# Kernel optimization log

Measured on AMD Instinct MI355X. Metric: run time of the kernel, lower is better.

## Reference

```python
import jax, jax.numpy as jnp
import numpy as np
from jax import lax

L = 2  # layer_nums (fixed per init_kwargs)

def setup_inputs() -> dict:
    key = jax.random.key(0)
    ks = jax.random.split(key, 8)
    B, T, V, E, U = 2048, 80, 10000, 100, 256
    tokens = jax.random.randint(ks[0], (B, T), 0, V, dtype=jnp.int32)
    emb = jax.random.normal(ks[1], (V, E), dtype=jnp.float32) * 0.05
    Wx0 = jax.random.normal(ks[2], (E, U), dtype=jnp.float32) * (1.0 / np.sqrt(E))
    Wx1 = jax.random.normal(ks[3], (U, U), dtype=jnp.float32) * (1.0 / np.sqrt(U))
    Wh = jax.random.normal(ks[4], (L, U, U), dtype=jnp.float32) * (1.0 / np.sqrt(U))
    b = jnp.zeros((L, U), dtype=jnp.float32)
    h0 = jax.random.uniform(ks[5], (L, B, U), dtype=jnp.float32)  # tf.random.uniform init states
    Wo = jax.random.normal(ks[6], (U, 1), dtype=jnp.float32) * (1.0 / np.sqrt(U))
    bo = jnp.zeros((1,), dtype=jnp.float32)
    return {"tokens": tokens, "emb": emb, "Wx0": Wx0, "Wx1": Wx1,
            "Wh": Wh, "b": b, "h0": h0, "Wo": Wo, "bo": bo}

def reference(tokens, emb, Wx0, Wx1, Wh, b, h0, Wo, bo):
    # Embedding lookup: [B, T] -> [B, T, E]
    x = emb[tokens]
    xT = jnp.swapaxes(x, 0, 1)  # [T, B, E] for time-major scan
    Wxs = [Wx0, Wx1]

    def step(h, xt):
        # h: [L, B, U]; xt: [B, E]
        inp = xt
        new_h = []
        for i in range(L):
            hi = jnp.tanh(inp @ Wxs[i] + h[i] @ Wh[i] + b[i])
            new_h.append(hi)
            inp = hi
        return jnp.stack(new_h), None

    hT, _ = lax.scan(step, h0, xT)
    out = hT[-1]                      # last layer's hidden at final timestep [B, U]
    z = out @ Wo + bo                 # Dense(1)
    return jax.nn.sigmoid(z)          # [B, 1]
```

## Files before the change

kernel.cpp:

```cpp
#include <hip/hip_runtime.h>
#include <hip/hip_bf16.h>

typedef __bf16 bf16x8 __attribute__((ext_vector_type(8)));
typedef __bf16 bf16x4 __attribute__((ext_vector_type(4)));
typedef float  f32x4  __attribute__((ext_vector_type(4)));

#define MFMA16(a,b,c) __builtin_amdgcn_mfma_f32_16x16x32_bf16((a),(b),(c),0,0,0)

#define PIN8(v8) do { f32x4 _t = __builtin_bit_cast(f32x4, (v8)); \
                      asm volatile("" : "+v"(_t)); \
                      (v8) = __builtin_bit_cast(bf16x8, _t); } while (0)

__device__ __forceinline__ void barrier_lds() {
  asm volatile("s_waitcnt lgkmcnt(0)\n\ts_barrier" ::: "memory");
}

constexpr int Bb = 2048, Tt = 80, Ee = 100, Uu = 256;
constexpr int BM = 8;
constexpr int RNT = 512;
constexpr int HCH = 256;
constexpr int HB = 8 * HCH;

template<bool ISBF>
__device__ __forceinline__ float ldf(const void* p, int i) {
  if constexpr (ISBF) return (float)((const __bf16*)p)[i];
  else                return ((const float*)p)[i];
}

__device__ __forceinline__ float fast_tanh(float x) {
  float e = __expf(2.f * x);
  return 1.f - 2.f / (e + 1.f);
}

__device__ __forceinline__ bool detect_bf16(const void* wh) {
  const unsigned short* u = (const unsigned short*)wh;
  int c = 0;
  const int lane = threadIdx.x & 63;
  #pragma unroll
  for (int r = 0; r < 4; ++r) {
    unsigned short h = u[2 * (lane + 64 * r)];
    int ex = (h >> 7) & 0xFF;
    if (ex >= 135 || (ex >= 1 && ex <= 95)) c++;
  }
  #pragma unroll
  for (int o = 32; o >= 1; o >>= 1) c += __shfl_down(c, o, 64);
  return __shfl(c, 0, 64) < 64;
}

template<bool ISBF>
__launch_bounds__(RNT, 2)
__global__ void rnn_kernel(const int* __restrict__ tokens,
                           const void* __restrict__ emb,
                           const void* __restrict__ Wx0,
                           const void* __restrict__ Wx1,
                           const void* __restrict__ Wh,
                           const void* __restrict__ bias,
                           const void* __restrict__ h0g,
                           const void* __restrict__ Wo,
                           const void* __restrict__ bo,
                           __bf16* __restrict__ U,
                           void* __restrict__ out) {
  if (detect_bf16(Wh) != ISBF) return;

  __shared__ __align__(16) __bf16 s_h0[2 * HB];
  __shared__ __align__(16) __bf16 s_h1[2 * HB];
  __shared__ int s_tok[BM * Tt];

  const int tid = threadIdx.x, lane = tid & 63, wv = tid >> 6;
  const int m = lane & 15, kc = lane >> 4, hf = lane >> 5;
  const int rb = blockIdx.x, b0 = rb * BM;
  const int au = (kc * 8 + (m & 7)) * 8;

  for (int idx = tid; idx < BM * Tt; idx += RNT)
    s_tok[idx] = tokens[b0 * Tt + idx];

  for (int idx = tid; idx < BM * Uu; idx += RNT) {
    int r = idx >> 8, c = idx & 255;
    int off = (c >> 5) * HCH + (((c >> 3) & 3) * 8 + r) * 8 + (c & 7);
    s_h0[off] = (__bf16)ldf<ISBF>(h0g, (b0 + r) * Uu + c);
    s_h1[off] = (__bf16)ldf<ISBF>(h0g, Bb * Uu + (b0 + r) * Uu + c);
  }
  __syncthreads();

  {
    bf16x8 fX[2][4];
    float b0v[2];
    #pragma unroll
    for (int e = 0; e < 2; ++e) {
      const int col = wv * 32 + e * 16 + m;
      b0v[e] = ldf<ISBF>(bias, col);
      #pragma unroll
      for (int s = 0; s < 4; ++s) {
        bf16x8 tr;
        #pragma unroll
        for (int j = 0; j < 8; ++j) {
          int k = s * 32 + kc * 8 + j;
          tr[j] = (k < Ee) ? (__bf16)ldf<ISBF>(Wx0, k * Uu + col) : (__bf16)0.f;
        }
        fX[e][s] = tr;
      }
    }
    const int tid32p = (wv >> 1) * 32 + (kc & 1) * 16 + m;
    __bf16* Ustore = U + (size_t)tid32p * 16 + (wv & 1) * 8;
    for (int tc = 0; tc < 10; ++tc) {
      const int T0 = tc * 8;
      bf16x8 xa[4][4];
      #pragma unroll
      for (int mt = 0; mt < 4; ++mt) {
        const int tok = s_tok[(m & 7) * Tt + T0 + mt * 2 + (m >> 3)];
        #pragma unroll
        for (int s = 0; s < 4; ++s) {
          const int k0 = s * 32 + kc * 8;
          if (k0 + 8 <= Ee) {
            if constexpr (ISBF) {
              xa[mt][s] = *(const bf16x8*)((const __bf16*)emb + tok * Ee + k0);
            } else {
              f32x4 lo = *(const f32x4*)((const float*)emb + tok * Ee + k0);
              f32x4 hi = *(const f32x4*)((const float*)emb + tok * Ee + k0 + 4);
              #pragma unroll
              for (int j = 0; j < 4; ++j) { xa[mt][s][j] = (__bf16)lo[j]; xa[mt][s][4 + j] = (__bf16)hi[j]; }
            }
          } else if (k0 < Ee) {
            if constexpr (ISBF) {
              bf16x4 t4 = *(const bf16x4*)((const __bf16*)emb + tok * Ee + k0);
              #pragma unroll
              for (int j = 0; j < 4; ++j) { xa[mt][s][j] = t4[j]; xa[mt][s][4 + j] = (__bf16)0.f; }
            } else {
              f32x4 t4 = *(const f32x4*)((const float*)emb + tok * Ee + k0);
              #pragma unroll
              for (int j = 0; j < 4; ++j) { xa[mt][s][j] = (__bf16)t4[j]; xa[mt][s][4 + j] = (__bf16)0.f; }
            }
          } else {
            #pragma unroll
            for (int j = 0; j < 8; ++j) xa[mt][s][j] = (__bf16)0.f;
          }
        }
      }
      #pragma unroll
      for (int mt = 0; mt < 4; ++mt) {
        f32x4 a0 = {b0v[0], b0v[0], b0v[0], b0v[0]};
        f32x4 a1 = {b0v[1], b0v[1], b0v[1], b0v[1]};
        #pragma unroll
        for (int s = 0; s < 4; ++s) {
          a0 = MFMA16(xa[mt][s], fX[0][s], a0);
          a1 = MFMA16(xa[mt][s], fX[1][s], a1);
        }
        bf16x8 pk;
        #pragma unroll
        for (int i = 0; i < 4; ++i) { pk[i] = (__bf16)a0[i]; pk[4 + i] = (__bf16)a1[i]; }
        const int t_l = T0 + mt * 2 + (kc >> 1);
        *(bf16x8*)(Ustore + (size_t)(t_l * 256 + rb) * 2048) = pk;
      }
    }
  }

  bf16x8 fWh0[2][8], fWx1f[2][8], fWh1[2][8];
  #pragma unroll
  for (int e = 0; e < 2; ++e) {
    const int col = wv * 32 + e * 16 + m;
    #pragma unroll
    for (int s = 0; s < 8; ++s) {
      const int kb = s * 32 + kc * 8;
      bf16x8 t0, t1, t2;
      #pragma unroll
      for (int j = 0; j < 8; ++j) {
        t0[j] = (__bf16)ldf<ISBF>(Wh,  (kb + j) * Uu + col);
        t1[j] = (__bf16)ldf<ISBF>(Wx1, (kb + j) * Uu + col);
        t2[j] = (__bf16)ldf<ISBF>(Wh,  Uu * Uu + (kb + j) * Uu + col);
      }
      fWh0[e][s] = t0; fWx1f[e][s] = t1; fWh1[e][s] = t2;
    }
  }
  #pragma unroll
  for (int e = 0; e < 2; ++e) {
    #pragma unroll
    for (int s = 0; s < 8; ++s) {
      PIN8(fWh0[e][s]); PIN8(fWx1f[e][s]); PIN8(fWh1[e][s]);
    }
  }
  const float b1s = ldf<ISBF>(bias, Uu + wv * 32 + hf * 16 + m);

  const int tid32u = (wv >> 1) * 32 + ((kc & 1) * 16) + m;
  const __bf16* Ubase = U + (size_t)tid32u * 16 + (wv & 1) * 8 + (size_t)rb * 2048;

  const int kc2 = m >> 3, j2 = m & 7, rgr = ((lane >> 4) & 1) * 4;
  const int toffw = wv * HCH + ((hf * 2 + kc2) * 8 + rgr) * 8 + j2;

  __syncthreads();

  bf16x8 u0 = *(const bf16x8*)(Ubase);

  {
    f32x4 d0 = {(float)u0[0], (float)u0[1], (float)u0[2], (float)u0[3]};
    f32x4 d1 = {(float)u0[4], (float)u0[5], (float)u0[6], (float)u0[7]};
    const __bf16* hb = s_h0 + au;
    #pragma unroll
    for (int s = 0; s < 8; ++s) {
      bf16x8 a = *(const bf16x8*)(hb + s * HCH);
      d0 = MFMA16(a, fWh0[0][s], d0);
      d1 = MFMA16(a, fWh0[1][s], d1);
    }
    u0 = *(const bf16x8*)(Ubase + (size_t)1 * 256 * 2048);
    __bf16* wp = s_h0 + HB + toffw;
    #pragma unroll
    for (int ii = 0; ii < 4; ++ii) {
      float dd = hf ? d1[ii] : d0[ii];
      wp[ii * 8] = (__bf16)fast_tanh(dd);
    }
    barrier_lds();
  }

  for (int t = 0; t < Tt; ++t) {
    const int p = t & 1, pn = p ^ 1;
    int tf = (t + 2 < Tt) ? t + 2 : Tt - 1;
    bf16x8 un = *(const bf16x8*)(Ubase + (size_t)tf * 256 * 2048);

    f32x4 cB0 = {0.f,0.f,0.f,0.f}, cB1 = {0.f,0.f,0.f,0.f};
    f32x4 cC0 = {0.f,0.f,0.f,0.f}, cC1 = {0.f,0.f,0.f,0.f};
    f32x4 cD0 = {(float)u0[0], (float)u0[1], (float)u0[2], (float)u0[3]};
    f32x4 cD1 = {(float)u0[4], (float)u0[5], (float)u0[6], (float)u0[7]};
    {
      const __bf16* h0b = s_h0 + pn * HB + au;
      const __bf16* h1b = s_h1 + p * HB + au;
      #pragma unroll
      for (int s = 0; s < 8; ++s) {
        bf16x8 a0 = *(const bf16x8*)(h0b + s * HCH);
        bf16x8 a1 = *(const bf16x8*)(h1b + s * HCH);
        cB0 = MFMA16(a0, fWx1f[0][s], cB0);
        cB1 = MFMA16(a0, fWx1f[1][s], cB1);
        cD0 = MFMA16(a0, fWh0[0][s], cD0);
        cD1 = MFMA16(a0, fWh0[1][s], cD1);
        cC0 = MFMA16(a1, fWh1[0][s], cC0);
        cC1 = MFMA16(a1, fWh1[1][s], cC1);
      }
    }
    {
      __bf16* wp1 = s_h1 + pn * HB + toffw;
      __bf16* wp0 = s_h0 + p * HB + toffw;
      #pragma unroll
      for (int ii = 0; ii < 4; ++ii) {
        float v1 = hf ? (cB1[ii] + cC1[ii]) : (cB0[ii] + cC0[ii]);
        float v0 = hf ? cD1[ii] : cD0[ii];
        wp1[ii * 8] = (__bf16)fast_tanh(v1 + b1s);
        wp0[ii * 8] = (__bf16)fast_tanh(v0);
      }
    }
    u0 = un;
    barrier_lds();
  }

  if (tid < 256) {
    const int r = tid >> 5, q = tid & 31;
    const __bf16* hp = s_h1 + (q >> 2) * HCH + ((q & 3) * 8 + r) * 8;
    bf16x8 hv = *(const bf16x8*)hp;
    float part = 0.f;
    #pragma unroll
    for (int j = 0; j < 8; ++j) part += (float)hv[j] * ldf<ISBF>(Wo, q * 8 + j);
    #pragma unroll
    for (int o = 16; o >= 1; o >>= 1) part += __shfl_down(part, o, 32);
    if (q == 0) {
      float z = part + ldf<ISBF>(bo, 0);
      float sg = 1.f / (1.f + __expf(-z));
      if constexpr (ISBF) ((__bf16*)out)[b0 + r] = (__bf16)sg;
      else                ((float*)out)[b0 + r]  = sg;
    }
  }
}

extern "C" void kernel_launch(void* const* d_in, const int* in_sizes, int n_in,
                              void* d_out, int out_size, void* d_ws, size_t ws_size,
                              hipStream_t stream) {
  const int*  tokens = (const int*)d_in[0];
  const void* emb = d_in[1];
  const void* Wx0 = d_in[2];
  const void* Wx1 = d_in[3];
  const void* Wh  = d_in[4];
  const void* b   = d_in[5];
  const void* h0  = d_in[6];
  const void* Wo  = d_in[7];
  const void* bo  = d_in[8];

  __bf16* U = (__bf16*)((char*)d_ws + 256);
  const size_t needU = 256 + (size_t)Tt * 256 * 2048 * sizeof(__bf16);
  if (ws_size < needU) return;

  rnn_kernel<true ><<<dim3(Bb / BM), dim3(RNT), 0, stream>>>(
      tokens, emb, Wx0, Wx1, Wh, b, h0, Wo, bo, U, d_out);
  rnn_kernel<false><<<dim3(Bb / BM), dim3(RNT), 0, stream>>>(
      tokens, emb, Wx0, Wx1, Wh, b, h0, Wo, bo, U, d_out);
}
```

Baseline: 243.1 us.

## Split recurrent step across 16 waves with permlane32 swap to combine partial results

Doubles the block to 1024 threads so each wave owns 16 output columns instead of 32, halving register-resident weight fragments per wave. Within a wave, lanes with m<8 and m>=8 read different hidden states (layer0 vs layer1). v_permlane32_swap exchanges the partial accumulators between half-waves so one half finalizes layer-1 and the other layer-0. This is meant to cut per-wave serial MFMA chain length and register pressure in the latency-bound recurrence. The cost is more waves per barrier, the extra permutes, and a runtime probe of permlane semantics.

New measurement: 333.5 us. 37.2% more time.

```diff
diff --git a/kernel.cpp b/kernel.cpp
--- a/kernel.cpp
+++ b/kernel.cpp
@@ -17,7 +17,7 @@
 
 constexpr int Bb = 2048, Tt = 80, Ee = 100, Uu = 256;
 constexpr int BM = 8;
-constexpr int RNT = 512;
+constexpr int RNT = 1024;
 constexpr int HCH = 256;
 constexpr int HB = 8 * HCH;
 
@@ -48,7 +48,7 @@
 }
 
 template<bool ISBF>
-__launch_bounds__(RNT, 2)
+__launch_bounds__(RNT)
 __global__ void rnn_kernel(const int* __restrict__ tokens,
                            const void* __restrict__ emb,
                            const void* __restrict__ Wx0,
@@ -68,8 +68,13 @@
 
   const int tid = threadIdx.x, lane = tid & 63, wv = tid >> 6;
   const int m = lane & 15, kc = lane >> 4, hf = lane >> 5;
+  const int mh = (m >> 3) & 1;
   const int rb = blockIdx.x, b0 = rb * BM;
-  const int au = (kc * 8 + (m & 7)) * 8;
+  const int au2 = (kc * 8 + (m & 7)) * 8;
+
+  int pv = lane, qv = 64 + lane;
+  asm volatile("v_permlane32_swap_b32 %0, %1" : "+v"(pv), "+v"(qv));
+  const bool forma = (__shfl(pv, 0, 64) == 0);
 
   for (int idx = tid; idx < BM * Tt; idx += RNT)
     s_tok[idx] = tokens[b0 * Tt + idx];
@@ -82,7 +87,7 @@
   }
   __syncthreads();
 
-  {
+  if (wv < 8) {
     bf16x8 fX[2][4];
     float b0v[2];
     #pragma unroll
@@ -154,10 +159,10 @@
     }
   }
 
-  bf16x8 fWh0[2][8], fWx1f[2][8], fWh1[2][8];
-  #pragma unroll
-  for (int e = 0; e < 2; ++e) {
-    const int col = wv * 32 + e * 16 + m;
+  const int tw = wv;
+  bf16x8 fWh0[8], fWx1f[8], fWh1[8];
+  {
+    const int col = tw * 16 + m;
     #pragma unroll
     for (int s = 0; s < 8; ++s) {
       const int kb = s * 32 + kc * 8;
@@ -168,44 +173,38 @@
         t1[j] = (__bf16)ldf<ISBF>(Wx1, (kb + j) * Uu + col);
         t2[j] = (__bf16)ldf<ISBF>(Wh,  Uu * Uu + (kb + j) * Uu + col);
       }
-      fWh0[e][s] = t0; fWx1f[e][s] = t1; fWh1[e][s] = t2;
+      fWh0[s] = t0; fWx1f[s] = t1; fWh1[s] = t2;
     }
   }
   #pragma unroll
-  for (int e = 0; e < 2; ++e) {
+  for (int s = 0; s < 8; ++s) { PIN8(fWh0[s]); PIN8(fWx1f[s]); PIN8(fWh1[s]); }
+
+  const float b1s = ldf<ISBF>(bias, Uu + tw * 16 + m);
+
+  const int O0u = (tw >> 2) * 512 + (kc & 1) * 256 + m * 16 +
+                  ((tw >> 1) & 1) * 8 + (tw & 1) * 4;
+  const __bf16* Ubase = U + (size_t)rb * 2048 + O0u;
+
+  const int woff = (tw >> 1) * 256 +
+                   ((((tw * 2) + (m >> 3)) & 3) * 8 + (kc & 1) * 4) * 8 + (m & 7);
+
+  __syncthreads();
+
+  bf16x4 u0 = *(const bf16x4*)(Ubase);
+
+  {
+    f32x4 d = {(float)u0[0], (float)u0[1], (float)u0[2], (float)u0[3]};
+    const __bf16* ab = (mh ? s_h1 : s_h0) + au2;
     #pragma unroll
     for (int s = 0; s < 8; ++s) {
-      PIN8(fWh0[e][s]); PIN8(fWx1f[e][s]); PIN8(fWh1[e][s]);
-    }
-  }
-  const float b1s = ldf<ISBF>(bias, Uu + wv * 32 + hf * 16 + m);
-
-  const int tid32u = (wv >> 1) * 32 + ((kc & 1) * 16) + m;
-  const __bf16* Ubase = U + (size_t)tid32u * 16 + (wv & 1) * 8 + (size_t)rb * 2048;
-
-  const int kc2 = m >> 3, j2 = m & 7, rgr = ((lane >> 4) & 1) * 4;
-  const int toffw = wv * HCH + ((hf * 2 + kc2) * 8 + rgr) * 8 + j2;
-
-  __syncthreads();
-
-  bf16x8 u0 = *(const bf16x8*)(Ubase);
-
-  {
-    f32x4 d0 = {(float)u0[0], (float)u0[1], (float)u0[2], (float)u0[3]};
-    f32x4 d1 = {(float)u0[4], (float)u0[5], (float)u0[6], (float)u0[7]};
-    const __bf16* hb = s_h0 + au;
-    #pragma unroll
-    for (int s = 0; s < 8; ++s) {
-      bf16x8 a = *(const bf16x8*)(hb + s * HCH);
-      d0 = MFMA16(a, fWh0[0][s], d0);
-      d1 = MFMA16(a, fWh0[1][s], d1);
-    }
-    u0 = *(const bf16x8*)(Ubase + (size_t)1 * 256 * 2048);
-    __bf16* wp = s_h0 + HB + toffw;
-    #pragma unroll
-    for (int ii = 0; ii < 4; ++ii) {
-      float dd = hf ? d1[ii] : d0[ii];
-      wp[ii * 8] = (__bf16)fast_tanh(dd);
+      bf16x8 a = *(const bf16x8*)(ab + s * HCH);
+      d = MFMA16(a, fWh0[s], d);
+    }
+    u0 = *(const bf16x4*)(Ubase + (size_t)1 * 256 * 2048);
+    if (hf == 0) {
+      __bf16* wp = s_h0 + HB + woff;
+      #pragma unroll
+      for (int ii = 0; ii < 4; ++ii) wp[ii * 8] = (__bf16)fast_tanh(d[ii]);
     }
     barrier_lds();
   }
@@ -213,37 +212,28 @@
   for (int t = 0; t < Tt; ++t) {
     const int p = t & 1, pn = p ^ 1;
     int tf = (t + 2 < Tt) ? t + 2 : Tt - 1;
-    bf16x8 un = *(const bf16x8*)(Ubase + (size_t)tf * 256 * 2048);
-
-    f32x4 cB0 = {0.f,0.f,0.f,0.f}, cB1 = {0.f,0.f,0.f,0.f};
-    f32x4 cC0 = {0.f,0.f,0.f,0.f}, cC1 = {0.f,0.f,0.f,0.f};
-    f32x4 cD0 = {(float)u0[0], (float)u0[1], (float)u0[2], (float)u0[3]};
-    f32x4 cD1 = {(float)u0[4], (float)u0[5], (float)u0[6], (float)u0[7]};
-    {
-      const __bf16* h0b = s_h0 + pn * HB + au;
-      const __bf16* h1b = s_h1 + p * HB + au;
-      #pragma unroll
-      for (int s = 0; s < 8; ++s) {
-        bf16x8 a0 = *(const bf16x8*)(h0b + s * HCH);
-        bf16x8 a1 = *(const bf16x8*)(h1b + s * HCH);
-        cB0 = MFMA16(a0, fWx1f[0][s], cB0);
-        cB1 = MFMA16(a0, fWx1f[1][s], cB1);
-        cD0 = MFMA16(a0, fWh0[0][s], cD0);
-        cD1 = MFMA16(a0, fWh0[1][s], cD1);
-        cC0 = MFMA16(a1, fWh1[0][s], cC0);
-        cC1 = MFMA16(a1, fWh1[1][s], cC1);
-      }
-    }
-    {
-      __bf16* wp1 = s_h1 + pn * HB + toffw;
-      __bf16* wp0 = s_h0 + p * HB + toffw;
-      #pragma unroll
-      for (int ii = 0; ii < 4; ++ii) {
-        float v1 = hf ? (cB1[ii] + cC1[ii]) : (cB0[ii] + cC0[ii]);
-        float v0 = hf ? cD1[ii] : cD0[ii];
-        wp1[ii * 8] = (__bf16)fast_tanh(v1 + b1s);
-        wp0[ii * 8] = (__bf16)fast_tanh(v0);
-      }
+    bf16x4 un = *(const bf16x4*)(Ubase + (size_t)tf * 256 * 2048);
+
+    const __bf16* ab = (mh ? (s_h1 + p * HB) : (s_h0 + pn * HB)) + au2;
+
+    f32x4 accX = {0.f, 0.f, 0.f, 0.f}, accH = {0.f, 0.f, 0.f, 0.f};
+    f32x4 accD = {(float)u0[0], (float)u0[1], (float)u0[2], (float)u0[3]};
+    #pragma unroll
+    for (int s = 0; s < 8; ++s) {
+      bf16x8 a = *(const bf16x8*)(ab + s * HCH);
+      accX = MFMA16(a, fWx1f[s], accX);
+      accH = MFMA16(a, fWh1[s], accH);
+      accD = MFMA16(a, fWh0[s], accD);
+    }
+
+    __bf16* wpw = (hf ? (s_h0 + p * HB) : (s_h1 + pn * HB)) + woff;
+    #pragma unroll
+    for (int i = 0; i < 4; ++i) {
+      float hx = accH[i], dx = accD[i];
+      if (forma) asm volatile("v_permlane32_swap_b32 %0, %1" : "+v"(hx), "+v"(dx));
+      else       asm volatile("v_permlane32_swap_b32 %0, %1" : "+v"(dx), "+v"(hx));
+      float v = hf ? hx : (accX[i] + dx + b1s);
+      wpw[i * 8] = (__bf16)fast_tanh(v);
     }
     u0 = un;
     barrier_lds();
```

## Split MFMA rows between h0/h1 sources and exchange results via permlane32 swap

Applied to the files above, without the earlier changes.

Each wave now uses the MFMA row dimension for both layers at once. Lanes with m<8 read the layer-0 hidden state and lanes with m>=8 read the layer-1 hidden state, so one LDS A-operand load per k-step feeds all six MFMAs instead of two separate loads. Partial results for the two layers are then exchanged between half-waves with v_permlane32_swap_b32, and each half-wave writes tanh outputs for one layer. This halves the LDS reads per step and balances the tanh/store work across lanes. In exchange it adds cross-lane swaps, a runtime probe of the swap semantics, and more complex index math.

Result: slower. 260.0 us (+7.0%).

```diff
diff --git a/kernel.cpp b/kernel.cpp
--- a/kernel.cpp
+++ b/kernel.cpp
@@ -68,8 +68,13 @@
 
   const int tid = threadIdx.x, lane = tid & 63, wv = tid >> 6;
   const int m = lane & 15, kc = lane >> 4, hf = lane >> 5;
+  const int mh = (m >> 3) & 1;
   const int rb = blockIdx.x, b0 = rb * BM;
-  const int au = (kc * 8 + (m & 7)) * 8;
+  const int au2 = (kc * 8 + (m & 7)) * 8;
+
+  int pv = lane, qv = 64 + lane;
+  asm volatile("v_permlane32_swap_b32 %0, %1" : "+v"(pv), "+v"(qv));
+  const bool forma = (__shfl(pv, 0, 64) == 0);
 
   for (int idx = tid; idx < BM * Tt; idx += RNT)
     s_tok[idx] = tokens[b0 * Tt + idx];
@@ -178,13 +183,19 @@
       PIN8(fWh0[e][s]); PIN8(fWx1f[e][s]); PIN8(fWh1[e][s]);
     }
   }
-  const float b1s = ldf<ISBF>(bias, Uu + wv * 32 + hf * 16 + m);
+  float b1v[2];
+  b1v[0] = ldf<ISBF>(bias, Uu + wv * 32 + m);
+  b1v[1] = ldf<ISBF>(bias, Uu + wv * 32 + 16 + m);
 
   const int tid32u = (wv >> 1) * 32 + ((kc & 1) * 16) + m;
   const __bf16* Ubase = U + (size_t)tid32u * 16 + (wv & 1) * 8 + (size_t)rb * 2048;
 
-  const int kc2 = m >> 3, j2 = m & 7, rgr = ((lane >> 4) & 1) * 4;
-  const int toffw = wv * HCH + ((hf * 2 + kc2) * 8 + rgr) * 8 + j2;
+  int woffe[2];
+  #pragma unroll
+  for (int e = 0; e < 2; ++e) {
+    const int col = (wv * 2 + e) * 16 + m;
+    woffe[e] = (col >> 5) * HCH + ((((col >> 3) & 3) * 8) + (kc & 1) * 4) * 8 + (col & 7);
+  }
 
   __syncthreads();
 
@@ -193,19 +204,20 @@
   {
     f32x4 d0 = {(float)u0[0], (float)u0[1], (float)u0[2], (float)u0[3]};
     f32x4 d1 = {(float)u0[4], (float)u0[5], (float)u0[6], (float)u0[7]};
-    const __bf16* hb = s_h0 + au;
+    const __bf16* ab = (mh ? s_h1 : s_h0) + au2;
     #pragma unroll
     for (int s = 0; s < 8; ++s) {
-      bf16x8 a = *(const bf16x8*)(hb + s * HCH);
+      bf16x8 a = *(const bf16x8*)(ab + s * HCH);
       d0 = MFMA16(a, fWh0[0][s], d0);
       d1 = MFMA16(a, fWh0[1][s], d1);
     }
     u0 = *(const bf16x8*)(Ubase + (size_t)1 * 256 * 2048);
-    __bf16* wp = s_h0 + HB + toffw;
-    #pragma unroll
-    for (int ii = 0; ii < 4; ++ii) {
-      float dd = hf ? d1[ii] : d0[ii];
-      wp[ii * 8] = (__bf16)fast_tanh(dd);
+    if (hf == 0) {
+      #pragma unroll
+      for (int ii = 0; ii < 4; ++ii) {
+        (s_h0 + HB + woffe[0])[ii * 8] = (__bf16)fast_tanh(d0[ii]);
+        (s_h0 + HB + woffe[1])[ii * 8] = (__bf16)fast_tanh(d1[ii]);
+      }
     }
     barrier_lds();
   }
@@ -215,35 +227,41 @@
     int tf = (t + 2 < Tt) ? t + 2 : Tt - 1;
     bf16x8 un = *(const bf16x8*)(Ubase + (size_t)tf * 256 * 2048);
 
-    f32x4 cB0 = {0.f,0.f,0.f,0.f}, cB1 = {0.f,0.f,0.f,0.f};
-    f32x4 cC0 = {0.f,0.f,0.f,0.f}, cC1 = {0.f,0.f,0.f,0.f};
-    f32x4 cD0 = {(float)u0[0], (float)u0[1], (float)u0[2], (float)u0[3]};
-    f32x4 cD1 = {(float)u0[4], (float)u0[5], (float)u0[6], (float)u0[7]};
-    {
-      const __bf16* h0b = s_h0 + pn * HB + au;
-      const __bf16* h1b = s_h1 + p * HB + au;
-      #pragma unroll
-      for (int s = 0; s < 8; ++s) {
-        bf16x8 a0 = *(const bf16x8*)(h0b + s * HCH);
-        bf16x8 a1 = *(const bf16x8*)(h1b + s * HCH);
-        cB0 = MFMA16(a0, fWx1f[0][s], cB0);
-        cB1 = MFMA16(a0, fWx1f[1][s], cB1);
-        cD0 = MFMA16(a0, fWh0[0][s], cD0);
-        cD1 = MFMA16(a0, fWh0[1][s], cD1);
-        cC0 = MFMA16(a1, fWh1[0][s], cC0);
-        cC1 = MFMA16(a1, fWh1[1][s], cC1);
-      }
-    }
-    {
-      __bf16* wp1 = s_h1 + pn * HB + toffw;
-      __bf16* wp0 = s_h0 + p * HB + toffw;
-      #pragma unroll
-      for (int ii = 0; ii < 4; ++ii) {
-        float v1 = hf ? (cB1[ii] + cC1[ii]) : (cB0[ii] + cC0[ii]);
-        float v0 = hf ? cD1[ii] : cD0[ii];
-        wp1[ii * 8] = (__bf16)fast_tanh(v1 + b1s);
-        wp0[ii * 8] = (__bf16)fast_tanh(v0);
-      }
+    const __bf16* ab = (mh ? (s_h1 + p * HB) : (s_h0 + pn * HB)) + au2;
+
+    f32x4 aX0 = {0.f,0.f,0.f,0.f}, aH0 = {0.f,0.f,0.f,0.f};
+    f32x4 aX1 = {0.f,0.f,0.f,0.f}, aH1 = {0.f,0.f,0.f,0.f};
+    f32x4 aD0 = {(float)u0[0], (float)u0[1], (float)u0[2], (float)u0[3]};
+    f32x4 aD1 = {(float)u0[4], (float)u0[5], (float)u0[6], (float)u0[7]};
+    #pragma unroll
+    for (int s = 0; s < 8; ++s) {
+      bf16x8 a = *(const bf16x8*)(ab + s * HCH);
+      aX0 = MFMA16(a, fWx1f[0][s], aX0);
+      aD0 = MFMA16(a, fWh0[0][s], aD0);
+      aH0 = MFMA16(a, fWh1[0][s], aH0);
+      aX1 = MFMA16(a, fWx1f[1][s], aX1);
+      aD1 = MFMA16(a, fWh0[1][s], aD1);
+      aH1 = MFMA16(a, fWh1[1][s], aH1);
+    }
+
+    __bf16* wb = hf ? (s_h0 + p * HB) : (s_h1 + pn * HB);
+    __bf16* wpw0 = wb + woffe[0];
+    __bf16* wpw1 = wb + woffe[1];
+    #pragma unroll
+    for (int i = 0; i < 4; ++i) {
+      float hx0 = aH0[i], dx0 = aD0[i];
+      float hx1 = aH1[i], dx1 = aD1[i];
+      if (forma) {
+        asm volatile("v_permlane32_swap_b32 %0, %1" : "+v"(hx0), "+v"(dx0));
+        asm volatile("v_permlane32_swap_b32 %0, %1" : "+v"(hx1), "+v"(dx1));
+      } else {
+        asm volatile("v_permlane32_swap_b32 %0, %1" : "+v"(dx0), "+v"(hx0));
+        asm volatile("v_permlane32_swap_b32 %0, %1" : "+v"(dx1), "+v"(hx1));
+      }
+      float v0 = hf ? hx0 : (aX0[i] + dx0 + b1v[0]);
+      float v1 = hf ? hx1 : (aX1[i] + dx1 + b1v[1]);
+      wpw0[i * 8] = (__bf16)fast_tanh(v0);
+      wpw1[i * 8] = (__bf16)fast_tanh(v1);
     }
     u0 = un;
     barrier_lds();
```
